# Optimization experiments

Hardware: AMD Instinct MI355X
Metric: run time of the kernel (lower is better)

The kernel has to match this reference:

```python
import jax, jax.numpy as jnp
import numpy as np

H = W = 56
WS = 7          # window size
SHIFT = 3       # shift size
HEADS = 4
DIM = 128
NUM_MLP = 512
EPS = 1e-5


def _build_rel_index():
    ch = np.arange(WS)
    cw = np.arange(WS)
    coords = np.stack(np.meshgrid(ch, cw, indexing='ij')).reshape(2, -1)  # [2,49]
    rel = coords[:, :, None] - coords[:, None, :]                         # [2,49,49]
    rel = rel.transpose(1, 2, 0)
    rel[:, :, 0] += WS - 1
    rel[:, :, 1] += WS - 1
    rel[:, :, 0] *= 2 * WS - 1
    return rel.sum(-1).astype(np.int32)                                   # [49,49]


def _build_attn_mask():
    mask = np.zeros((H, W), dtype=np.float32)
    slices = (slice(0, -WS), slice(-WS, -SHIFT), slice(-SHIFT, None))
    cnt = 0
    for hs in slices:
        for ws_ in slices:
            mask[hs, ws_] = cnt
            cnt += 1
    nH, nW = H // WS, W // WS
    mw = mask.reshape(nH, WS, nW, WS).transpose(0, 2, 1, 3).reshape(nH * nW, WS * WS)
    am = mw[:, None, :] - mw[:, :, None]
    return np.where(am != 0, -100.0, 0.0).astype(np.float32)              # [64,49,49]


def setup_inputs() -> dict:
    key = jax.random.key(0)
    ks = jax.random.split(key, 8)
    B = 64
    s = 0.02
    return {
        'x': jax.random.normal(ks[0], (B, H * W, DIM), jnp.float32),
        'ln1_g': jnp.ones((DIM,), jnp.float32),
        'ln1_b': jnp.zeros((DIM,), jnp.float32),
        'eca_w': jax.random.normal(ks[1], (3, DIM, 1), jnp.float32) * s,
        'qkv_w': jax.random.normal(ks[2], (DIM, 3 * DIM), jnp.float32) * s,
        'qkv_b': jnp.zeros((3 * DIM,), jnp.float32),
        'rel_bias_table': jax.random.normal(ks[3], ((2 * WS - 1) ** 2, HEADS), jnp.float32) * s,
        'proj_w': jax.random.normal(ks[4], (DIM, DIM), jnp.float32) * s,
        'proj_b': jnp.zeros((DIM,), jnp.float32),
        'ln2_g': jnp.ones((DIM,), jnp.float32),
        'ln2_b': jnp.zeros((DIM,), jnp.float32),
        'mlp_w1': jax.random.normal(ks[5], (DIM, NUM_MLP), jnp.float32) * s,
        'mlp_b1': jnp.zeros((NUM_MLP,), jnp.float32),
        'mlp_w2': jax.random.normal(ks[6], (NUM_MLP, DIM), jnp.float32) * s,
        'mlp_b2': jnp.zeros((DIM,), jnp.float32),
        'attn_mask': jnp.asarray(_build_attn_mask()),
        'rel_index': jnp.asarray(_build_rel_index()),
    }


def _layer_norm(x, g, b):
    mu = x.mean(-1, keepdims=True)
    var = jnp.mean((x - mu) ** 2, -1, keepdims=True)
    return (x - mu) * jax.lax.rsqrt(var + EPS) * g + b


def _forward(x, ln1_g, ln1_b, eca_w, qkv_w, qkv_b, rel_bias_table, proj_w, proj_b,
             ln2_g, ln2_b, mlp_w1, mlp_b1, mlp_w2, mlp_b2, attn_mask, rel_index):
    B, L, C = x.shape
    nH, nW = H // WS, W // WS
    nwin = nH * nW
    hd = C // HEADS
    scale = hd ** -0.5

    x_skip = x
    xs = _layer_norm(x, ln1_g, ln1_b)
    x4 = xs.reshape(B, H, W, C)

    # Efficient channel attention (faithful: Conv1D over a length-1 steps axis,
    # 'same' padding -> only the center kernel tap contributes; gate is [B,1,1])
    sq = x4.mean((1, 2))[:, None, :]                                  # [B,1,C]
    gate = jax.lax.conv_general_dilated(
        sq, eca_w, (1,), 'SAME', dimension_numbers=('NWC', 'WIO', 'NWC'))  # [B,1,1]
    gate = jax.nn.sigmoid(gate)
    cattn = (x4 * gate[:, :, :, None]).reshape(B, H * W, C)

    # cyclic shift + window partition (batch-major, standard Swin layout)
    shifted = jnp.roll(x4, (-SHIFT, -SHIFT), (1, 2))
    xw = shifted.reshape(B, nH, WS, nW, WS, C).transpose(0, 1, 3, 2, 4, 5)
    xw = xw.reshape(B * nwin, WS * WS, C)                              # [Bn,49,C]

    # window attention with gathered relative position bias
    qkv = (xw @ qkv_w + qkv_b).reshape(-1, WS * WS, 3, HEADS, hd)
    qkv = qkv.transpose(2, 0, 3, 1, 4)                                 # [3,Bn,h,49,hd]
    q, k, v = qkv[0], qkv[1], qkv[2]
    attn = jnp.einsum('bhqd,bhkd->bhqk', q * scale, k)                 # [Bn,h,49,49]
    bias = rel_bias_table[rel_index.reshape(-1)]                       # [49*49,h]
    bias = bias.reshape(WS * WS, WS * WS, HEADS).transpose(2, 0, 1)    # [h,49,49]
    attn = attn + bias[None]
    attn = attn.reshape(B, nwin, HEADS, WS * WS, WS * WS) + attn_mask[None, :, None]
    attn = jax.nn.softmax(attn.reshape(-1, HEADS, WS * WS, WS * WS), -1)
    out = jnp.einsum('bhqk,bhkd->bqhd', attn, v).reshape(-1, WS * WS, C)
    out = out @ proj_w + proj_b                                        # [Bn,49,C]

    # window reverse + reverse shift
    out = out.reshape(B, nH, nW, WS, WS, C).transpose(0, 1, 3, 2, 4, 5)
    out = out.reshape(B, H, W, C)
    out = jnp.roll(out, (SHIFT, SHIFT), (1, 2)).reshape(B, H * W, C)

    x = x_skip + out + cattn
    x_skip = x
    xn = _layer_norm(x, ln2_g, ln2_b)
    h1 = jax.nn.gelu(xn @ mlp_w1 + mlp_b1, approximate=False)
    return x_skip + (h1 @ mlp_w2 + mlp_b2)


def reference(x, ln1_g, ln1_b, eca_w, qkv_w, qkv_b, rel_bias_table, proj_w, proj_b,
              ln2_g, ln2_b, mlp_w1, mlp_b1, mlp_w2, mlp_b2, attn_mask, rel_index):
    return _forward(x, ln1_g, ln1_b, eca_w, qkv_w, qkv_b, rel_bias_table, proj_w,
                    proj_b, ln2_g, ln2_b, mlp_w1, mlp_b1, mlp_w2, mlp_b2,
                    attn_mask, rel_index)
```

## Files before the change

kernel.cpp:

```cpp
#include <hip/hip_runtime.h>
#include <hip/hip_bf16.h>
#include <math.h>

#define B_    64
#define Himg  56
#define Wimg  56
#define L_    (Himg*Wimg)
#define WS_   7
#define SHIFT 3
#define NWIN  64
#define NTOK  49
#define HEADS 4
#define HD    32
#define DIM   128
#define NMLP  512
#define EPS   1e-5f
#define SCALE 0.17677669529663687f

typedef __hip_bfloat16 bf16;
typedef __attribute__((ext_vector_type(8))) short short8;
typedef __attribute__((ext_vector_type(4))) float floatx4;
typedef __attribute__((ext_vector_type(4))) int intx4;
typedef __attribute__((ext_vector_type(4))) unsigned short ushort4v;
#define MFMA16(a, b, c) __builtin_amdgcn_mfma_f32_16x16x32_bf16(a, b, c, 0, 0, 0)

__device__ float g_gacc[B_];
__device__ __align__(16) unsigned short g_w1t[NMLP * DIM];
__device__ __align__(16) unsigned short g_w2t[DIM * NMLP];
__device__ __align__(16) unsigned short g_qkvwt[3 * DIM * DIM];
__device__ __align__(16) unsigned short g_pwt[DIM * DIM];
__device__ float g_combo[NWIN * HEADS * NTOK * NTOK];

__device__ __forceinline__ float us2f(unsigned short u) {
  return __uint_as_float(((unsigned int)u) << 16);
}
__device__ __forceinline__ unsigned short f2us(float f) {
  unsigned int x = __float_as_uint(f);
  x += 0x7fffu + ((x >> 16) & 1u);
  return (unsigned short)(x >> 16);
}
__device__ __forceinline__ bool is_bf(const void* ones) {
  return ((const unsigned int*)ones)[0] == 0x3F803F80u;
}
template<bool BF>
__device__ __forceinline__ float ldf(const void* p, size_t i) {
  if (BF) return __bfloat162float(((const bf16*)p)[i]);
  return ((const float*)p)[i];
}
template<bool BF>
__device__ __forceinline__ floatx4 ld4(const void* p, size_t i) {
  if (BF) {
    const ushort4v u = *(const ushort4v*)((const unsigned short*)p + i);
    floatx4 r = {us2f(u.x), us2f(u.y), us2f(u.z), us2f(u.w)};
    return r;
  }
  return *(const floatx4*)((const float*)p + i);
}
template<bool BF>
__device__ __forceinline__ void st4(void* p, size_t i, floatx4 v) {
  if (BF) {
    ushort4v u = {f2us(v.x), f2us(v.y), f2us(v.z), f2us(v.w)};
    *(ushort4v*)((unsigned short*)p + i) = u;
  } else {
    *(floatx4*)((float*)p + i) = v;
  }
}
__device__ __forceinline__ float gelu_t(float x) {
  float y = 0.7978845608028654f * (x + 0.044715f * x * x * x);
  y = fminf(fmaxf(y, -15.f), 15.f);
  const float e = __expf(2.f * y);
  return 0.5f * x * (1.f + (e - 1.f) / (e + 1.f));
}

template<bool BF>
__global__ void k_prep(const void* __restrict__ w1, const void* __restrict__ w2,
                       const void* __restrict__ qkvw, const void* __restrict__ pw,
                       const void* __restrict__ rbt, const void* __restrict__ amask,
                       const int* __restrict__ ridx, const void* __restrict__ ones) {
  if (is_bf(ones) != BF) return;
  const int bid = blockIdx.x, tid = threadIdx.x;
  if (bid == 0 && tid < B_) g_gacc[tid] = 0.f;
  if (bid < 256) {
    const int idx = bid * 256 + tid;
    { const int k = idx >> 9, n = idx & 511; g_w1t[n * DIM + k] = f2us(ldf<BF>(w1, idx)); }
    { const int k = idx >> 7, n = idx & 127; g_w2t[n * NMLP + k] = f2us(ldf<BF>(w2, idx)); }
  } else if (bid < 448) {
    const int idx = (bid - 256) * 256 + tid;
    { const int k = idx / 384, n = idx % 384; g_qkvwt[n * DIM + k] = f2us(ldf<BF>(qkvw, idx)); }
    if (idx < DIM * DIM) {
      const int k = idx >> 7, n = idx & 127;
      g_pwt[n * DIM + k] = f2us(ldf<BF>(pw, idx));
    }
  } else {
    const int wh_ = bid - 448;
    const int widx = wh_ >> 2, h = wh_ & 3;
    for (int idx = tid; idx < NTOK * NTOK; idx += 256) {
      const int jj = idx / NTOK, ii = idx - jj * NTOK;
      g_combo[(size_t)wh_ * (NTOK * NTOK) + idx] =
          ldf<BF>(rbt, (size_t)ridx[ii * NTOK + jj] * HEADS + h) +
          ldf<BF>(amask, (size_t)widx * (NTOK * NTOK) + ii * NTOK + jj);
    }
  }
}

template<bool BF>
__global__ void k_gate_partial(const void* __restrict__ x,
                               const void* __restrict__ ln1_g,
                               const void* __restrict__ ln1_b,
                               const void* __restrict__ eca_w) {
  if (is_bf(ln1_g) != BF) return;
  const int b = blockIdx.x;
  const int lane = threadIdx.x & 63;
  const int wave = threadIdx.x >> 6;
  const int c4 = (lane & 31) * 4;
  const floatx4 g4  = ld4<BF>(ln1_g, c4);
  const floatx4 be4 = ld4<BF>(ln1_b, c4);
  const floatx4 w4  = ld4<BF>(eca_w, DIM + c4);
  float acc = 0.f;
  const int t0 = blockIdx.y * 8 + wave * 2 + (lane >> 5);
  for (int t = t0; t < L_; t += 256) {
    const floatx4 v = ld4<BF>(x, ((size_t)b * L_ + t) * DIM + c4);
    float s = v.x + v.y + v.z + v.w;
    float s2 = v.x * v.x + v.y * v.y + v.z * v.z + v.w * v.w;
    #pragma unroll
    for (int m = 1; m <= 16; m <<= 1) {
      s  += __shfl_xor(s,  m, 64);
      s2 += __shfl_xor(s2, m, 64);
    }
    const float mu = s * (1.f / DIM);
    const float rs = rsqrtf(s2 * (1.f / DIM) - mu * mu + EPS);
    acc += ((v.x - mu) * rs * g4.x + be4.x) * w4.x
         + ((v.y - mu) * rs * g4.y + be4.y) * w4.y
         + ((v.z - mu) * rs * g4.z + be4.z) * w4.z
         + ((v.w - mu) * rs * g4.w + be4.w) * w4.w;
  }
  #pragma unroll
  for (int m = 1; m <= 32; m <<= 1) acc += __shfl_xor(acc, m, 64);
  if (lane == 0) atomicAdd(&g_gacc[b], acc);
}

template<bool BF>
__global__ __launch_bounds__(512, 4) void k_attn_mfma(
    const void* __restrict__ x,
    const void* __restrict__ ln1_g, const void* __restrict__ ln1_b,
    const void* __restrict__ qkv_b, const void* __restrict__ proj_b,
    void* __restrict__ x2) {
  if (is_bf(ln1_g) != BF) return;
  __shared__ __align__(16) unsigned short q_s[NTOK * 136];
  __shared__ __align__(16) unsigned short k_s[NTOK * 136];
  __shared__ __align__(16) unsigned short xno[NTOK * 136];
  __shared__ __align__(16) unsigned short vt[128 * 72];
  __shared__ float mu[NTOK], rs[NTOK];
  __shared__ int off_s[NTOK];
  unsigned short* o_s = q_s;

  const int tid = threadIdx.x;
  const int bw = blockIdx.x;
  const int b = bw >> 6, widx = bw & 63;
  const int wh = widx >> 3, wc = widx & 7;
  const int w = tid >> 6, l = tid & 63;
  const int pair = w >> 1, p = w & 1;
  const int lr = l & 15, lq = l >> 4;

  {
    const int i = tid >> 3, j = tid & 7;
    if (i < NTOK) {
      const int r = i / 7, qq = i % 7;
      const int oh = (wh * 7 + r + SHIFT) % Himg;
      const int ow = (wc * 7 + qq + SHIFT) % Wimg;
      const int sp = oh * Wimg + ow;
      if (j == 0) off_s[i] = sp;
      const size_t base = ((size_t)b * L_ + sp) * DIM;
      const int c0 = j * 16;
      const floatx4 v0 = ld4<BF>(x, base + c0);
      const floatx4 v1 = ld4<BF>(x, base + c0 + 4);
      const floatx4 v2 = ld4<BF>(x, base + c0 + 8);
      const floatx4 v3 = ld4<BF>(x, base + c0 + 12);
      float s = v0.x + v0.y + v0.z + v0.w + v1.x + v1.y + v1.z + v1.w
              + v2.x + v2.y + v2.z + v2.w + v3.x + v3.y + v3.z + v3.w;
      float s2 = v0.x * v0.x + v0.y * v0.y + v0.z * v0.z + v0.w * v0.w
               + v1.x * v1.x + v1.y * v1.y + v1.z * v1.z + v1.w * v1.w
               + v2.x * v2.x + v2.y * v2.y + v2.z * v2.z + v2.w * v2.w
               + v3.x * v3.x + v3.y * v3.y + v3.z * v3.z + v3.w * v3.w;
      s  += __shfl_xor(s, 1, 64);  s  += __shfl_xor(s, 2, 64);  s  += __shfl_xor(s, 4, 64);
      s2 += __shfl_xor(s2, 1, 64); s2 += __shfl_xor(s2, 2, 64); s2 += __shfl_xor(s2, 4, 64);
      const float m = s * (1.f / DIM);
      const float rr = rsqrtf(s2 * (1.f / DIM) - m * m + EPS);
      if (j == 0) { mu[i] = m; rs[i] = rr; }
      const floatx4 g0 = ld4<BF>(ln1_g, c0),     g1 = ld4<BF>(ln1_g, c0 + 4);
      const floatx4 g2 = ld4<BF>(ln1_g, c0 + 8), g3 = ld4<BF>(ln1_g, c0 + 12);
      const floatx4 e0 = ld4<BF>(ln1_b, c0),     e1 = ld4<BF>(ln1_b, c0 + 4);
      const floatx4 e2 = ld4<BF>(ln1_b, c0 + 8), e3 = ld4<BF>(ln1_b, c0 + 12);
      short8 o0, o1;
      o0[0] = (short)f2us((v0.x - m) * rr * g0.x + e0.x);
      o0[1] = (short)f2us((v0.y - m) * rr * g0.y + e0.y);
      o0[2] = (short)f2us((v0.z - m) * rr * g0.z + e0.z);
      o0[3] = (short)f2us((v0.w - m) * rr * g0.w + e0.w);
      o0[4] = (short)f2us((v1.x - m) * rr * g1.x + e1.x);
      o0[5] = (short)f2us((v1.y - m) * rr * g1.y + e1.y);
      o0[6] = (short)f2us((v1.z - m) * rr * g1.z + e1.z);
      o0[7] = (short)f2us((v1.w - m) * rr * g1.w + e1.w);
      o1[0] = (short)f2us((v2.x - m) * rr * g2.x + e2.x);
      o1[1] = (short)f2us((v2.y - m) * rr * g2.y + e2.y);
      o1[2] = (short)f2us((v2.z - m) * rr * g2.z + e2.z);
      o1[3] = (short)f2us((v2.w - m) * rr * g2.w + e2.w);
      o1[4] = (short)f2us((v3.x - m) * rr * g3.x + e3.x);
      o1[5] = (short)f2us((v3.y - m) * rr * g3.y + e3.y);
      o1[6] = (short)f2us((v3.z - m) * rr * g3.z + e3.z);
      o1[7] = (short)f2us((v3.w - m) * rr * g3.w + e3.w);
      *(short8*)&xno[i * 136 + c0] = o0;
      *(short8*)&xno[i * 136 + c0 + 8] = o1;
    } else {
      const short8 zz = {0, 0, 0, 0, 0, 0, 0, 0};
      for (int z = tid - NTOK * 8; z < 256; z += 512 - NTOK * 8) {
        const int d = z >> 1, o = (z & 1) * 8;
        *(short8*)&vt[d * 72 + 48 + o] = zz;
      }
    }
  }
  __syncthreads();

  {
    const int mp = p;
    for (int np = 0; np < 3; np++) {
      const int n0 = pair * 96 + np * 32 + lr;
      const int n1 = n0 + 16;
      floatx4 a00 = {0.f, 0.f, 0.f, 0.f}, a01 = a00, a10 = a00, a11 = a00;
      #pragma unroll
      for (int kc = 0; kc < 4; kc++) {
        const int k0 = kc * 32 + lq * 8;
        const short8 A0 = *(const short8*)&xno[(mp * 32 + lr) * 136 + k0];
        const short8 A1 = *(const short8*)&xno[(mp * 32 + 16 + lr) * 136 + k0];
        const short8 B0 = *(const short8*)&g_qkvwt[n0 * DIM + k0];
        const short8 B1 = *(const short8*)&g_qkvwt[n1 * DIM + k0];
        a00 = MFMA16(A0, B0, a00); a01 = MFMA16(A0, B1, a01);
        a10 = MFMA16(A1, B0, a10); a11 = MFMA16(A1, B1, a11);
      }
      const float bb0 = ldf<BF>(qkv_b, n0), bb1 = ldf<BF>(qkv_b, n1);
      #pragma unroll
      for (int r = 0; r < 4; r++) {
        const int i0 = mp * 32 + lq * 4 + r, i1 = i0 + 16;
        #pragma unroll
        for (int t = 0; t < 4; t++) {
          const int i = (t & 2) ? i1 : i0;
          const int n = (t & 1) ? n1 : n0;
          const float val = (t == 0 ? a00[r] : t == 1 ? a01[r] : t == 2 ? a10[r] : a11[r])
                            + ((t & 1) ? bb1 : bb0);
          if (i < NTOK) {
            const unsigned short hv = f2us(val);
            if (n < DIM) q_s[i * 136 + n] = hv;
            else if (n < 2 * DIM) k_s[i * 136 + (n - DIM)] = hv;
            else vt[(n - 2 * DIM) * 72 + i] = hv;
          }
        }
      }
    }
  }
  __syncthreads();

  {
    const int h = pair;
    const size_t cbase = (size_t)((widx << 2) + h) * (NTOK * NTOK);
    short8 Ak[4], Av[4];
    #pragma unroll
    for (int ni = 0; ni < 4; ni++)
      Ak[ni] = *(const short8*)&k_s[(ni * 16 + lr) * 136 + h * 32 + lq * 8];
    #pragma unroll
    for (int half = 0; half < 2; half++)
      #pragma unroll
      for (int kq = 0; kq < 2; kq++)
        Av[half * 2 + kq] =
            *(const short8*)&vt[(h * 32 + half * 16 + lr) * 72 + kq * 32 + lq * 8];

    const int s0lane = (l & 15) | ((l & 16) << 1);
    const int s1lane = s0lane + 16;
    const bool selhi = (l >> 5) & 1;

    for (int mm = 0; mm < 2; mm++) {
      const int mi = p * 2 + mm;
      const int iq = mi * 16 + lr;
      const short8 Bq = *(const short8*)&q_s[iq * 136 + h * 32 + lq * 8];
      float sv[4][4];
      #pragma unroll
      for (int ni = 0; ni < 4; ni++) {
        floatx4 z = {0.f, 0.f, 0.f, 0.f};
        const floatx4 sc = MFMA16(Ak[ni], Bq, z);
        #pragma unroll
        for (int r = 0; r < 4; r++) {
          const int j = ni * 16 + lq * 4 + r;
          float s = -1e30f;
          if (iq < NTOK && j < NTOK)
            s = sc[r] * SCALE + g_combo[cbase + j * NTOK + iq];
          sv[ni][r] = s;
        }
      }
      float m0 = fmaxf(fmaxf(sv[0][0], sv[0][1]), fmaxf(sv[0][2], sv[0][3]));
      float m1 = fmaxf(fmaxf(sv[1][0], sv[1][1]), fmaxf(sv[1][2], sv[1][3]));
      float m2 = fmaxf(fmaxf(sv[2][0], sv[2][1]), fmaxf(sv[2][2], sv[2][3]));
      float m3 = fmaxf(fmaxf(sv[3][0], sv[3][1]), fmaxf(sv[3][2], sv[3][3]));
      float mx = fmaxf(fmaxf(m0, m1), fmaxf(m2, m3));
      mx = fmaxf(mx, __shfl_xor(mx, 16, 64));
      mx = fmaxf(mx, __shfl_xor(mx, 32, 64));
      float ss = 0.f;
      #pragma unroll
      for (int ni = 0; ni < 4; ni++) {
        #pragma unroll
        for (int r = 0; r < 4; r++) { sv[ni][r] = __expf(sv[ni][r] - mx); }
        ss += (sv[ni][0] + sv[ni][1]) + (sv[ni][2] + sv[ni][3]);
      }
      ss += __shfl_xor(ss, 16, 64);
      ss += __shfl_xor(ss, 32, 64);
      const float inv = 1.f / ss;
      int pk_lo[4], pk_hi[4];
      #pragma unroll
      for (int ni = 0; ni < 4; ni++) {
        pk_lo[ni] = (int)((unsigned)f2us(sv[ni][0] * inv) |
                          ((unsigned)f2us(sv[ni][1] * inv) << 16));
        pk_hi[ni] = (int)((unsigned)f2us(sv[ni][2] * inv) |
                          ((unsigned)f2us(sv[ni][3] * inv) << 16));
      }
      floatx4 oc0 = {0.f, 0.f, 0.f, 0.f}, oc1 = oc0;
      #pragma unroll
      for (int kq = 0; kq < 2; kq++) {
        const int a_lo0 = __shfl(pk_lo[2 * kq],     s0lane, 64);
        const int a_lo1 = __shfl(pk_lo[2 * kq + 1], s0lane, 64);
        const int a_hi0 = __shfl(pk_hi[2 * kq],     s0lane, 64);
        const int a_hi1 = __shfl(pk_hi[2 * kq + 1], s0lane, 64);
        const int b_lo0 = __shfl(pk_lo[2 * kq],     s1lane, 64);
        const int b_lo1 = __shfl(pk_lo[2 * kq + 1], s1lane, 64);
        const int b_hi0 = __shfl(pk_hi[2 * kq],     s1lane, 64);
        const int b_hi1 = __shfl(pk_hi[2 * kq + 1], s1lane, 64);
        intx4 t;
        t.x = selhi ? a_lo1 : a_lo0;
        t.y = selhi ? a_hi1 : a_hi0;
        t.z = selhi ? b_lo1 : b_lo0;
        t.w = selhi ? b_hi1 : b_hi0;
        const short8 Bp = *(const short8*)&t;
        oc0 = MFMA16(Av[kq], Bp, oc0);
        oc1 = MFMA16(Av[2 + kq], Bp, oc1);
      }
      if (iq < NTOK) {
        #pragma unroll
        for (int r = 0; r < 4; r++) {
          xno[iq * 136 + h * 32 + lq * 4 + r]      = f2us(oc0[r]);
          xno[iq * 136 + h * 32 + 16 + lq * 4 + r] = f2us(oc1[r]);
        }
      }
    }
  }
  __syncthreads();

  {
    const int mp = p;
    const int n0 = pair * 32 + lr, n1 = n0 + 16;
    floatx4 a00 = {0.f, 0.f, 0.f, 0.f}, a01 = a00, a10 = a00, a11 = a00;
    #pragma unroll
    for (int kc = 0; kc < 4; kc++) {
      const int k0 = kc * 32 + lq * 8;
      const short8 A0 = *(const short8*)&xno[(mp * 32 + lr) * 136 + k0];
      const short8 A1 = *(const short8*)&xno[(mp * 32 + 16 + lr) * 136 + k0];
      const short8 B0 = *(const short8*)&g_pwt[n0 * DIM + k0];
      const short8 B1 = *(const short8*)&g_pwt[n1 * DIM + k0];
      a00 = MFMA16(A0, B0, a00); a01 = MFMA16(A0, B1, a01);
      a10 = MFMA16(A1, B0, a10); a11 = MFMA16(A1, B1, a11);
    }
    const float pb0 = ldf<BF>(proj_b, n0), pb1 = ldf<BF>(proj_b, n1);
    #pragma unroll
    for (int r = 0; r < 4; r++) {
      const int i0 = mp * 32 + lq * 4 + r, i1 = i0 + 16;
      if (i0 < NTOK) {
        o_s[i0 * 136 + n0] = f2us(a00[r] + pb0);
        o_s[i0 * 136 + n1] = f2us(a01[r] + pb1);
      }
      if (i1 < NTOK) {
        o_s[i1 * 136 + n0] = f2us(a10[r] + pb0);
        o_s[i1 * 136 + n1] = f2us(a11[r] + pb1);
      }
    }
  }
  __syncthreads();
  {
    const float gb = 1.f / (1.f + __expf(-g_gacc[b] * (1.f / (float)L_)));
    for (int idx = tid; idx < NTOK * 32; idx += 512) {
      const int i = idx >> 5, c4 = (idx & 31) * 4;
      const size_t pos = ((size_t)b * L_ + off_s[i]) * DIM + c4;
      const floatx4 xv = ld4<BF>(x, pos);
      const ushort4v o4 = *(const ushort4v*)&o_s[i * 136 + c4];
      const floatx4 g4 = ld4<BF>(ln1_g, c4);
      const floatx4 b4 = ld4<BF>(ln1_b, c4);
      const float m = mu[i], rr = rs[i];
      floatx4 out;
      out.x = xv.x + us2f(o4.x) + gb * ((xv.x - m) * rr * g4.x + b4.x);
      out.y = xv.y + us2f(o4.y) + gb * ((xv.y - m) * rr * g4.y + b4.y);
      out.z = xv.z + us2f(o4.z) + gb * ((xv.z - m) * rr * g4.z + b4.z);
      out.w = xv.w + us2f(o4.w) + gb * ((xv.w - m) * rr * g4.w + b4.w);
      st4<BF>(x2, pos, out);
    }
  }
}

template<bool BF>
__global__ __launch_bounds__(512, 6) void k_mlp_mfma(
    const void* __restrict__ ln2_g, const void* __restrict__ ln2_b,
    const void* __restrict__ b1v, const void* __restrict__ b2v,
    void* __restrict__ io) {
  if (is_bf(ln2_g) != BF) return;
  __shared__ __align__(16) unsigned short xn[64][136];
  __shared__ __align__(16) unsigned short h1[64][264];
  const int tid = threadIdx.x;
  const size_t t0 = (size_t)blockIdx.x * 64;
  const int w = tid >> 6, l = tid & 63;
  const int lr = l & 15, lq = l >> 4;

  {
    const int i = tid >> 3, c0 = (tid & 7) * 16;
    const size_t base = (t0 + i) * DIM + c0;
    const floatx4 va = ld4<BF>(io, base);
    const floatx4 vb = ld4<BF>(io, base + 4);
    const floatx4 vc = ld4<BF>(io, base + 8);
    const floatx4 vd = ld4<BF>(io, base + 12);
    float s = va.x + va.y + va.z + va.w + vb.x + vb.y + vb.z + vb.w
            + vc.x + vc.y + vc.z + vc.w + vd.x + vd.y + vd.z + vd.w;
    float s2 = va.x * va.x + va.y * va.y + va.z * va.z + va.w * va.w
             + vb.x * vb.x + vb.y * vb.y + vb.z * vb.z + vb.w * vb.w
             + vc.x * vc.x + vc.y * vc.y + vc.z * vc.z + vc.w * vc.w
             + vd.x * vd.x + vd.y * vd.y + vd.z * vd.z + vd.w * vd.w;
    s  += __shfl_xor(s, 1, 64);  s  += __shfl_xor(s, 2, 64);  s  += __shfl_xor(s, 4, 64);
    s2 += __shfl_xor(s2, 1, 64); s2 += __shfl_xor(s2, 2, 64); s2 += __shfl_xor(s2, 4, 64);
    const float m = s * (1.f / DIM);
    const float rr = rsqrtf(s2 * (1.f / DIM) - m * m + EPS);
    const floatx4 g0 = ld4<BF>(ln2_g, c0),     g1 = ld4<BF>(ln2_g, c0 + 4);
    const floatx4 g2 = ld4<BF>(ln2_g, c0 + 8), g3 = ld4<BF>(ln2_g, c0 + 12);
    const floatx4 e0 = ld4<BF>(ln2_b, c0),     e1 = ld4<BF>(ln2_b, c0 + 4);
    const floatx4 e2 = ld4<BF>(ln2_b, c0 + 8), e3 = ld4<BF>(ln2_b, c0 + 12);
    short8 o0, o1;
    o0[0] = (short)f2us((va.x - m) * rr * g0.x + e0.x);
    o0[1] = (short)f2us((va.y - m) * rr * g0.y + e0.y);
    o0[2] = (short)f2us((va.z - m) * rr * g0.z + e0.z);
    o0[3] = (short)f2us((va.w - m) * rr * g0.w + e0.w);
    o0[4] = (short)f2us((vb.x - m) * rr * g1.x + e1.x);
    o0[5] = (short)f2us((vb.y - m) * rr * g1.y + e1.y);
    o0[6] = (short)f2us((vb.z - m) * rr * g1.z + e1.z);
    o0[7] = (short)f2us((vb.w - m) * rr * g1.w + e1.w);
    o1[0] = (short)f2us((vc.x - m) * rr * g2.x + e2.x);
    o1[1] = (short)f2us((vc.y - m) * rr * g2.y + e2.y);
    o1[2] = (short)f2us((vc.z - m) * rr * g2.z + e2.z);
    o1[3] = (short)f2us((vc.w - m) * rr * g2.w + e2.w);
    o1[4] = (short)f2us((vd.x - m) * rr * g3.x + e3.x);
    o1[5] = (short)f2us((vd.y - m) * rr * g3.y + e3.y);
    o1[6] = (short)f2us((vd.z - m) * rr * g3.z + e3.z);
    o1[7] = (short)f2us((vd.w - m) * rr * g3.w + e3.w);
    *(short8*)&xn[i][c0] = o0;
    *(short8*)&xn[i][c0 + 8] = o1;
  }
  __syncthreads();

  floatx4 c2[4] = {{0.f, 0.f, 0.f, 0.f}, {0.f, 0.f, 0.f, 0.f},
                   {0.f, 0.f, 0.f, 0.f}, {0.f, 0.f, 0.f, 0.f}};

  #pragma unroll
  for (int half = 0; half < 2; half++) {
    {
      const int n0 = half * 256 + w * 32 + lr;
      const int n1 = n0 + 16;
      floatx4 a0[4] = {{0.f, 0.f, 0.f, 0.f}, {0.f, 0.f, 0.f, 0.f},
                       {0.f, 0.f, 0.f, 0.f}, {0.f, 0.f, 0.f, 0.f}};
      floatx4 a1[4] = {{0.f, 0.f, 0.f, 0.f}, {0.f, 0.f, 0.f, 0.f},
                       {0.f, 0.f, 0.f, 0.f}, {0.f, 0.f, 0.f, 0.f}};
      #pragma unroll
      for (int kc = 0; kc < 4; kc++) {
        const int k0 = kc * 32 + lq * 8;
        const short8 B0 = *(const short8*)&g_w1t[n0 * DIM + k0];
        const short8 B1 = *(const short8*)&g_w1t[n1 * DIM + k0];
        #pragma unroll
        for (int mt = 0; mt < 4; mt++) {
          const short8 A = *(const short8*)&xn[mt * 16 + lr][k0];
          a0[mt] = MFMA16(A, B0, a0[mt]);
          a1[mt] = MFMA16(A, B1, a1[mt]);
        }
      }
      const float bb0 = ldf<BF>(b1v, n0);
      const float bb1 = ldf<BF>(b1v, n1);
      const int hc0 = w * 32 + lr;
      #pragma unroll
      for (int mt = 0; mt < 4; mt++) {
        #pragma unroll
        for (int r = 0; r < 4; r++) {
          const int row = mt * 16 + lq * 4 + r;
          h1[row][hc0]      = f2us(gelu_t(a0[mt][r] + bb0));
          h1[row][hc0 + 16] = f2us(gelu_t(a1[mt][r] + bb1));
        }
      }
    }
    __syncthreads();

    {
      const int nc = w * 16 + lr;
      const int kb = half * 256;
      #pragma unroll
      for (int kc = 0; kc < 8; kc++) {
        const int k0 = kc * 32 + lq * 8;
        const short8 B = *(const short8*)&g_w2t[nc * NMLP + kb + k0];
        #pragma unroll
        for (int mt = 0; mt < 4; mt++) {
          const short8 A = *(const short8*)&h1[mt * 16 + lr][k0];
          c2[mt] = MFMA16(A, B, c2[mt]);
        }
      }
    }
    __syncthreads();
  }

  {
    const int nc = w * 16 + lr;
    const float bb = ldf<BF>(b2v, nc);
    #pragma unroll
    for (int mt = 0; mt < 4; mt++) {
      #pragma unroll
      for (int r = 0; r < 4; r++) {
        const int row = mt * 16 + lq * 4 + r;
        xn[row][nc] = f2us(c2[mt][r] + bb);
      }
    }
  }
  __syncthreads();

  for (int idx = tid; idx < 64 * 32; idx += 512) {
    const int i = idx >> 5, c4 = (idx & 31) * 4;
    const size_t pos = (t0 + i) * DIM + c4;
    const floatx4 v = ld4<BF>(io, pos);
    const ushort4v o4 = *(const ushort4v*)&xn[i][c4];
    floatx4 out = {v.x + us2f(o4.x), v.y + us2f(o4.y),
                   v.z + us2f(o4.z), v.w + us2f(o4.w)};
    st4<BF>(io, pos, out);
  }
}

extern "C" void kernel_launch(void* const* d_in, const int* in_sizes, int n_in,
                              void* d_out, int out_size, void* d_ws, size_t ws_size,
                              hipStream_t stream) {
  const void* x     = d_in[0];
  const void* ln1g  = d_in[1];
  const void* ln1b  = d_in[2];
  const void* ecaw  = d_in[3];
  const void* qkvw  = d_in[4];
  const void* qkvb  = d_in[5];
  const void* rbt   = d_in[6];
  const void* projw = d_in[7];
  const void* projb = d_in[8];
  const void* ln2g  = d_in[9];
  const void* ln2b  = d_in[10];
  const void* w1    = d_in[11];
  const void* b1    = d_in[12];
  const void* w2    = d_in[13];
  const void* b2    = d_in[14];
  const void* amask = d_in[15];
  const int*  ridx  = (const int*)d_in[16];

  const int gsz = in_sizes[1];
  const bool launch_bf = (gsz != 512);
  const bool launch_fp = (gsz != 256);

  if (launch_bf) k_prep<true ><<<704, 256, 0, stream>>>(w1, w2, qkvw, projw, rbt, amask, ridx, ln1g);
  if (launch_fp) k_prep<false><<<704, 256, 0, stream>>>(w1, w2, qkvw, projw, rbt, amask, ridx, ln1g);
  if (launch_bf) k_gate_partial<true ><<<dim3(B_, 32), 256, 0, stream>>>(x, ln1g, ln1b, ecaw);
  if (launch_fp) k_gate_partial<false><<<dim3(B_, 32), 256, 0, stream>>>(x, ln1g, ln1b, ecaw);
  if (launch_bf) k_attn_mfma<true ><<<B_ * NWIN, 512, 0, stream>>>(x, ln1g, ln1b, qkvb, projb, d_out);
  if (launch_fp) k_attn_mfma<false><<<B_ * NWIN, 512, 0, stream>>>(x, ln1g, ln1b, qkvb, projb, d_out);
  if (launch_bf) k_mlp_mfma<true ><<<(B_ * L_) / 64, 512, 0, stream>>>(ln2g, ln2b, b1, b2, d_out);
  if (launch_fp) k_mlp_mfma<false><<<(B_ * L_) / 64, 512, 0, stream>>>(ln2g, ln2b, b1, b2, d_out);
}
```

Measured before the change: 594.5 us.

## Drop q_s shared buffer, swizzle V transpose, raise attention kernel occupancy

Removes the separate Q shared-memory buffer by holding Q in registers during the QKV GEMM and writing it into the xno buffer once LayerNorm output is no longer needed. The projection output now reuses k_s. The transposed V buffer loses its padding and uses an XOR-swizzled index to avoid bank conflicts. Launch bounds are raised from 4 to 6 blocks per CU to exploit the smaller LDS footprint. The cost is an extra barrier, added register pressure from holding Q, and possible spills under the tighter register limit.

```diff
diff --git a/kernel.cpp b/kernel.cpp
--- a/kernel.cpp
+++ b/kernel.cpp
@@ -70,6 +70,9 @@
   y = fminf(fmaxf(y, -15.f), 15.f);
   const float e = __expf(2.f * y);
   return 0.5f * x * (1.f + (e - 1.f) / (e + 1.f));
+}
+__device__ __forceinline__ int vtix(int d, int tok) {
+  return d * 64 + (tok ^ ((d & 7) << 3));
 }
 
 template<bool BF>
@@ -140,19 +143,18 @@
 }
 
 template<bool BF>
-__global__ __launch_bounds__(512, 4) void k_attn_mfma(
+__global__ __launch_bounds__(512, 6) void k_attn_mfma(
     const void* __restrict__ x,
     const void* __restrict__ ln1_g, const void* __restrict__ ln1_b,
     const void* __restrict__ qkv_b, const void* __restrict__ proj_b,
     void* __restrict__ x2) {
   if (is_bf(ln1_g) != BF) return;
-  __shared__ __align__(16) unsigned short q_s[NTOK * 136];
   __shared__ __align__(16) unsigned short k_s[NTOK * 136];
   __shared__ __align__(16) unsigned short xno[NTOK * 136];
-  __shared__ __align__(16) unsigned short vt[128 * 72];
+  __shared__ __align__(16) unsigned short vt[128 * 64];
   __shared__ float mu[NTOK], rs[NTOK];
   __shared__ int off_s[NTOK];
-  unsigned short* o_s = q_s;
+  unsigned short* o_s = k_s;
 
   const int tid = threadIdx.x;
   const int bw = blockIdx.x;
@@ -162,6 +164,10 @@
   const int pair = w >> 1, p = w & 1;
   const int lr = l & 15, lq = l >> 4;
 
+  for (int idx = tid; idx < 128 * 16; idx += 512) {
+    const int d = idx >> 4, t = 48 + (idx & 15);
+    vt[vtix(d, t)] = 0;
+  }
   {
     const int i = tid >> 3, j = tid & 7;
     if (i < NTOK) {
@@ -210,20 +216,17 @@
       o1[7] = (short)f2us((v3.w - m) * rr * g3.w + e3.w);
       *(short8*)&xno[i * 136 + c0] = o0;
       *(short8*)&xno[i * 136 + c0 + 8] = o1;
-    } else {
-      const short8 zz = {0, 0, 0, 0, 0, 0, 0, 0};
-      for (int z = tid - NTOK * 8; z < 256; z += 512 - NTOK * 8) {
-        const int d = z >> 1, o = (z & 1) * 8;
-        *(short8*)&vt[d * 72 + 48 + o] = zz;
-      }
     }
   }
   __syncthreads();
 
+  floatx4 q00, q01, q10, q11;
   {
     const int mp = p;
-    for (int np = 0; np < 3; np++) {
-      const int n0 = pair * 96 + np * 32 + lr;
+    const int nc = pair * 32 + lr;
+    #pragma unroll
+    for (int np = 2; np >= 0; np--) {
+      const int n0 = np * 128 + nc;
       const int n1 = n0 + 16;
       floatx4 a00 = {0.f, 0.f, 0.f, 0.f}, a01 = a00, a10 = a00, a11 = a00;
       #pragma unroll
@@ -237,22 +240,55 @@
         a10 = MFMA16(A1, B0, a10); a11 = MFMA16(A1, B1, a11);
       }
       const float bb0 = ldf<BF>(qkv_b, n0), bb1 = ldf<BF>(qkv_b, n1);
-      #pragma unroll
-      for (int r = 0; r < 4; r++) {
-        const int i0 = mp * 32 + lq * 4 + r, i1 = i0 + 16;
-        #pragma unroll
-        for (int t = 0; t < 4; t++) {
-          const int i = (t & 2) ? i1 : i0;
-          const int n = (t & 1) ? n1 : n0;
-          const float val = (t == 0 ? a00[r] : t == 1 ? a01[r] : t == 2 ? a10[r] : a11[r])
-                            + ((t & 1) ? bb1 : bb0);
-          if (i < NTOK) {
-            const unsigned short hv = f2us(val);
-            if (n < DIM) q_s[i * 136 + n] = hv;
-            else if (n < 2 * DIM) k_s[i * 136 + (n - DIM)] = hv;
-            else vt[(n - 2 * DIM) * 72 + i] = hv;
+      if (np == 0) {
+        #pragma unroll
+        for (int r = 0; r < 4; r++) {
+          q00[r] = a00[r] + bb0; q01[r] = a01[r] + bb1;
+          q10[r] = a10[r] + bb0; q11[r] = a11[r] + bb1;
+        }
+      } else if (np == 1) {
+        #pragma unroll
+        for (int r = 0; r < 4; r++) {
+          const int i0 = mp * 32 + lq * 4 + r, i1 = i0 + 16;
+          if (i0 < NTOK) {
+            k_s[i0 * 136 + nc]      = f2us(a00[r] + bb0);
+            k_s[i0 * 136 + nc + 16] = f2us(a01[r] + bb1);
           }
-        }
+          if (i1 < NTOK) {
+            k_s[i1 * 136 + nc]      = f2us(a10[r] + bb0);
+            k_s[i1 * 136 + nc + 16] = f2us(a11[r] + bb1);
+          }
+        }
+      } else {
+        #pragma unroll
+        for (int r = 0; r < 4; r++) {
+          const int i0 = mp * 32 + lq * 4 + r, i1 = i0 + 16;
+          if (i0 < NTOK) {
+            vt[vtix(nc, i0)]      = f2us(a00[r] + bb0);
+            vt[vtix(nc + 16, i0)] = f2us(a01[r] + bb1);
+          }
+          if (i1 < NTOK) {
+            vt[vtix(nc, i1)]      = f2us(a10[r] + bb0);
+            vt[vtix(nc + 16, i1)] = f2us(a11[r] + bb1);
+          }
+        }
+      }
+    }
+  }
+  __syncthreads();
+  {
+    const int mp = p;
+    const int nc = pair * 32 + lr;
+    #pragma unroll
+    for (int r = 0; r < 4; r++) {
+      const int i0 = mp * 32 + lq * 4 + r, i1 = i0 + 16;
+      if (i0 < NTOK) {
+        xno[i0 * 136 + nc]      = f2us(q00[r]);
+        xno[i0 * 136 + nc + 16] = f2us(q01[r]);
+      }
+      if (i1 < NTOK) {
+        xno[i1 * 136 + nc]      = f2us(q10[r]);
+        xno[i1 * 136 + nc + 16] = f2us(q11[r]);
       }
     }
   }
@@ -268,9 +304,10 @@
     #pragma unroll
     for (int half = 0; half < 2; half++)
       #pragma unroll
-      for (int kq = 0; kq < 2; kq++)
-        Av[half * 2 + kq] =
-            *(const short8*)&vt[(h * 32 + half * 16 + lr) * 72 + kq * 32 + lq * 8];
+      for (int kq = 0; kq < 2; kq++) {
+        const int d = h * 32 + half * 16 + lr;
+        Av[half * 2 + kq] = *(const short8*)&vt[vtix(d, kq * 32 + lq * 8)];
+      }
 
     const int s0lane = (l & 15) | ((l & 16) << 1);
     const int s1lane = s0lane + 16;
@@ -279,7 +316,7 @@
     for (int mm = 0; mm < 2; mm++) {
       const int mi = p * 2 + mm;
       const int iq = mi * 16 + lr;
-      const short8 Bq = *(const short8*)&q_s[iq * 136 + h * 32 + lq * 8];
+      const short8 Bq = *(const short8*)&xno[iq * 136 + h * 32 + lq * 8];
       float sv[4][4];
       #pragma unroll
       for (int ni = 0; ni < 4; ni++) {
@@ -365,6 +402,7 @@
       a10 = MFMA16(A1, B0, a10); a11 = MFMA16(A1, B1, a11);
     }
     const float pb0 = ldf<BF>(proj_b, n0), pb1 = ldf<BF>(proj_b, n1);
+    __syncthreads();
     #pragma unroll
     for (int r = 0; r < 4; r++) {
       const int i0 = mp * 32 + lq * 4 + r, i1 = i0 + 16;
```

Measured after the change: 580.3 us. -2.4%, faster.
